# Kernel optimization log

Measured on AMD Instinct MI355X. Metric: run time of the kernel, lower is better.

The kernel has to match this reference:

```python
import jax, jax.numpy as jnp
import numpy as np

D_MODEL = 1024
N_HEADS = 16
N_GROUPS = 4
D_HEAD = D_MODEL // N_HEADS  # 64
HPG = N_HEADS // N_GROUPS    # heads per KV group = 4
B, T = 2, 2048


def _rope(x):
    # x: [B, H, T, D]; interleaved even/odd rotary, matching the torch module
    t, d = x.shape[2], x.shape[3]
    pos = jnp.arange(t, dtype=jnp.float32)[:, None]                      # [T,1]
    freq = jnp.exp(-(jnp.arange(0, d, 2, dtype=jnp.float32) / d)
                   * jnp.log(jnp.float32(10000.0)))                      # [D/2]
    angle = pos * freq                                                   # [T, D/2]
    cos, sin = jnp.cos(angle), jnp.sin(angle)
    xe, xo = x[..., ::2], x[..., 1::2]
    re = xe * cos - xo * sin
    ro = xe * sin + xo * cos
    return jnp.stack([re, ro], axis=-1).reshape(x.shape)


def setup_inputs() -> dict:
    key = jax.random.key(0)
    ks = jax.random.split(key, 10)
    s = 0.02
    return {
        "x":  jax.random.normal(ks[0], (B, T, D_MODEL), dtype=jnp.float32),
        "Wq": jax.random.normal(ks[1], (D_MODEL, D_MODEL), dtype=jnp.float32) * s,
        "bq": jax.random.normal(ks[2], (D_MODEL,), dtype=jnp.float32) * s,
        "Wk": jax.random.normal(ks[3], (D_MODEL, N_GROUPS * D_HEAD), dtype=jnp.float32) * s,
        "bk": jax.random.normal(ks[4], (N_GROUPS * D_HEAD,), dtype=jnp.float32) * s,
        "Wv": jax.random.normal(ks[5], (D_MODEL, N_GROUPS * D_HEAD), dtype=jnp.float32) * s,
        "bv": jax.random.normal(ks[6], (N_GROUPS * D_HEAD,), dtype=jnp.float32) * s,
        "Wo": jax.random.normal(ks[7], (D_MODEL, D_MODEL), dtype=jnp.float32) * s,
        "bo": jax.random.normal(ks[8], (D_MODEL,), dtype=jnp.float32) * s,
    }


def reference(x, Wq, bq, Wk, bk, Wv, bv, Wo, bo):
    b, t, _ = x.shape
    q = (x @ Wq + bq).reshape(b, t, N_HEADS, D_HEAD).transpose(0, 2, 1, 3)    # [B,H,T,D]
    k = (x @ Wk + bk).reshape(b, t, N_GROUPS, D_HEAD).transpose(0, 2, 1, 3)   # [B,G,T,D]
    v = (x @ Wv + bv).reshape(b, t, N_GROUPS, D_HEAD).transpose(0, 2, 1, 3)
    # GQA broadcast: idx = arange(n_heads) // heads_per_group  ==  repeat each group HPG times
    k = jnp.repeat(k, HPG, axis=1)                                            # [B,H,T,D]
    v = jnp.repeat(v, HPG, axis=1)
    q = _rope(q)
    k = _rope(k)
    scale = jnp.float32(np.sqrt(D_HEAD))
    scores = jnp.einsum('bhtd,bhsd->bhts', q, k) / scale                      # [B,H,T,T]
    causal = jnp.tril(jnp.ones((t, t), dtype=bool))
    scores = jnp.where(causal, scores, -jnp.inf)
    probs = jax.nn.softmax(scores, axis=-1)
    # dropout(p=0.05) is identity in eval mode
    attn = jnp.einsum('bhts,bhsd->bhtd', probs, v)
    out = attn.transpose(0, 2, 1, 3).reshape(b, t, N_HEADS * D_HEAD)
    return out @ Wo + bo
```

## Files before the change

### kernel.cpp

```cpp
#include <hip/hip_runtime.h>
#include <stdint.h>

typedef unsigned short u16;
typedef __attribute__((ext_vector_type(4))) float f32x4;
typedef __attribute__((ext_vector_type(8))) short bf16x8;
typedef __attribute__((ext_vector_type(4))) short bf16x4;

#define T_SEQ 2048
#define DM 1024
#define NH 16
#define NG 4
#define DH 64
#define QSCALE 0.18033688011112042f

__device__ __forceinline__ u16 f2bf(float f) {
    union { float f; uint32_t u; } v; v.f = f;
    uint32_t r = (v.u + 0x7FFFu + ((v.u >> 16) & 1u)) >> 16;
    return (u16)r;
}
__device__ __forceinline__ float bf2f(u16 u) {
    union { uint32_t u; float f; } v; v.u = ((uint32_t)u) << 16;
    return v.f;
}
__device__ __forceinline__ float fexp2(float x) {
#if __has_builtin(__builtin_amdgcn_exp2f)
    return __builtin_amdgcn_exp2f(x);
#else
    return exp2f(x);
#endif
}
__device__ __forceinline__ uint32_t cvtpk_bf16(float a, float b) {
    uint32_t r;
    asm("v_cvt_pk_bf16_f32 %0, %1, %2" : "=v"(r) : "v"(a), "v"(b));
    return r;
}

#if __has_builtin(__builtin_amdgcn_mfma_f32_16x16x16_bf16)
__device__ __forceinline__ f32x4 mfma16(bf16x4 a, bf16x4 b, f32x4 c) {
    return __builtin_amdgcn_mfma_f32_16x16x16_bf16(a, b, c, 0, 0, 0);
}
#elif __has_builtin(__builtin_amdgcn_mfma_f32_16x16x16bf16_1k)
__device__ __forceinline__ f32x4 mfma16(bf16x4 a, bf16x4 b, f32x4 c) {
    return __builtin_amdgcn_mfma_f32_16x16x16bf16_1k(a, b, c, 0, 0, 0);
}
#else
__device__ __forceinline__ f32x4 mfma16(bf16x4 a, bf16x4 b, f32x4 c) {
    asm("v_mfma_f32_16x16x16_bf16 %0, %1, %2, %0" : "+v"(c) : "v"(a), "v"(b));
    return c;
}
#endif

__device__ __forceinline__ void async16(const void* g, void* l) {
    __builtin_amdgcn_global_load_lds(
        (const __attribute__((address_space(1))) void*)g,
        (__attribute__((address_space(3))) void*)l,
        16, 0, 0);
}

__global__ __launch_bounds__(256) void k_prep(
    const float* __restrict__ x, u16* __restrict__ xb,
    const float* __restrict__ Wq, const float* __restrict__ Wk,
    const float* __restrict__ Wv, const float* __restrict__ Wo,
    u16* __restrict__ wqkvt, u16* __restrict__ wot,
    const float* __restrict__ bq, const float* __restrict__ bk,
    const float* __restrict__ bv, float* __restrict__ bqkv,
    float2* __restrict__ tbl) {
    int blk = blockIdx.x;
    int tid = threadIdx.x;
    if (blk < 2048) {
        int i = blk * 256 + tid;
        const float4* p = (const float4*)x + (size_t)i * 2;
        float4 a = p[0], b = p[1];
        bf16x8 v;
        v[0] = (short)f2bf(a.x); v[1] = (short)f2bf(a.y);
        v[2] = (short)f2bf(a.z); v[3] = (short)f2bf(a.w);
        v[4] = (short)f2bf(b.x); v[5] = (short)f2bf(b.y);
        v[6] = (short)f2bf(b.z); v[7] = (short)f2bf(b.w);
        ((bf16x8*)xb)[i] = v;
        return;
    }
    int t = blk - 2048;
    if (t >= 2560) {
        int u = t - 2560;
        if (u < 6) {
            int i = u * 256 + tid;
            if (i < 1536) {
                float v;
                if (i < 1024) v = bq[i];
                else if (i < 1280) v = bk[i - 1024];
                else v = bv[i - 1280];
                bqkv[i] = v;
            }
        } else {
            int idx = (u - 6) * 256 + tid;
            int tt = idx >> 5, i = idx & 31;
            float freq = exp2f(-(float)i * (13.287712379549449f / 32.0f));
            float ang = (float)tt * freq;
            tbl[idx] = make_float2(cosf(ang), sinf(ang));
        }
        return;
    }
    const float* src; u16* dst; int N;
    if (t < 1024)      { src = Wq; dst = wqkvt;                      N = 1024; }
    else if (t < 1280) { t -= 1024; src = Wk; dst = wqkvt + (size_t)1024 * 1024; N = 256; }
    else if (t < 1536) { t -= 1280; src = Wv; dst = wqkvt + (size_t)1280 * 1024; N = 256; }
    else               { t -= 1536; src = Wo; dst = wot;             N = 1024; }
    int ntiles = N >> 5;
    int n0 = (t % ntiles) * 32, k0 = (t / ntiles) * 32;
    __shared__ float tile[32][33];
    int tx = tid & 31, ty = tid >> 5;
#pragma unroll
    for (int q = 0; q < 4; q++)
        tile[ty + q * 8][tx] = src[(size_t)(k0 + ty + q * 8) * N + n0 + tx];
    __syncthreads();
#pragma unroll
    for (int q = 0; q < 4; q++)
        dst[(size_t)(n0 + ty + q * 8) * 1024 + k0 + tx] = f2bf(tile[tx][ty + q * 8]);
}

template <int B16OUT>
__global__ __launch_bounds__(256) void k_gemm_bt(
    const u16* __restrict__ A, const u16* __restrict__ Bt,
    const float* __restrict__ bias, void* __restrict__ Cv,
    int M, int N, int K) {
    __shared__ __align__(16) u16 As[64 * 64];
    __shared__ __align__(16) u16 Bs[128 * 64];
    int tid = threadIdx.x;
    int lane = tid & 63, wid = tid >> 6;
    int wr = wid >> 1, wc = wid & 1;
    int l15 = lane & 15, lhi = lane >> 4;
    int row0 = blockIdx.y * 64, col0 = blockIdx.x * 128;
    f32x4 acc[2][4] = {};

    for (int k0 = 0; k0 < K; k0 += 64) {
#pragma unroll
        for (int i = 0; i < 2; i++) {
            int c = i * 256 + tid;
            int r = c >> 3, ch = c & 7;
            int sch = ch ^ (r & 7);
            async16(A + (size_t)(row0 + r) * K + k0 + sch * 8, &As[c * 8]);
        }
#pragma unroll
        for (int i = 0; i < 4; i++) {
            int c = i * 256 + tid;
            int r = c >> 3, ch = c & 7;
            int sch = ch ^ (r & 7);
            async16(Bt + (size_t)(col0 + r) * K + k0 + sch * 8, &Bs[c * 8]);
        }
        __syncthreads();
#pragma unroll
        for (int ks = 0; ks < 2; ks++) {
            bf16x8 af[2], bfr[4];
#pragma unroll
            for (int m = 0; m < 2; m++) {
                int r = wr * 32 + m * 16 + l15;
                int kb = (ks * 64 + lhi * 16) ^ ((r & 7) << 4);
                af[m] = *(const bf16x8*)((const char*)As + r * 128 + kb);
            }
#pragma unroll
            for (int n = 0; n < 4; n++) {
                int r = wc * 64 + n * 16 + l15;
                int kb = (ks * 64 + lhi * 16) ^ ((r & 7) << 4);
                bfr[n] = *(const bf16x8*)((const char*)Bs + r * 128 + kb);
            }
#pragma unroll
            for (int m = 0; m < 2; m++)
#pragma unroll
                for (int n = 0; n < 4; n++)
                    acc[m][n] = __builtin_amdgcn_mfma_f32_16x16x32_bf16(
                        af[m], bfr[n], acc[m][n], 0, 0, 0);
        }
        __syncthreads();
    }
#pragma unroll
    for (int n = 0; n < 4; n++) {
        int col = col0 + wc * 64 + n * 16 + l15;
        float bv = bias[col];
#pragma unroll
        for (int m = 0; m < 2; m++) {
            int row = row0 + wr * 32 + m * 16 + lhi * 4;
#pragma unroll
            for (int i = 0; i < 4; i++) {
                float v = acc[m][n][i] + bv;
                if (B16OUT) ((u16*)Cv)[(size_t)(row + i) * N + col] = f2bf(v);
                else        ((float*)Cv)[(size_t)(row + i) * N + col] = v;
            }
        }
    }
}

__global__ __launch_bounds__(256) void k_rope_scatter(
    const u16* __restrict__ qkv, const float2* __restrict__ tbl,
    u16* __restrict__ Qo, u16* __restrict__ Ko, u16* __restrict__ Vto) {
    int bt = blockIdx.x;
    int t = bt & (T_SEQ - 1), b = bt >> 11;
    const u16* row = qkv + (size_t)bt * 1536;
    const uint32_t* row32 = (const uint32_t*)row;
    __shared__ float cs[32], sn[32];
    int tid = threadIdx.x;
    if (tid < 32) {
        float2 p = tbl[t * 32 + tid];
        cs[tid] = p.x; sn[tid] = p.y;
    }
    __syncthreads();
    for (int j = tid; j < 512; j += 256) {
        int i = j & 31;
        uint32_t w = row32[j];
        float xe = bf2f((u16)w), xo = bf2f((u16)(w >> 16));
        float c = cs[i], s = sn[i];
        float re = (xe * c - xo * s) * QSCALE;
        float ro = (xe * s + xo * c) * QSCALE;
        int hq = j >> 5;
        size_t base = (((size_t)(b * NH + hq)) * T_SEQ + t) * DH + 2 * i;
        Qo[base] = f2bf(re); Qo[base + 1] = f2bf(ro);
    }
    if (tid < 128) {
        int g = tid >> 5, i = tid & 31;
        uint32_t w = row32[512 + tid];
        float xe = bf2f((u16)w), xo = bf2f((u16)(w >> 16));
        float c = cs[i], s = sn[i];
        float re = xe * c - xo * s;
        float ro = xe * s + xo * c;
        size_t base = (((size_t)(b * NG + g)) * T_SEQ + t) * DH + 2 * i;
        Ko[base] = f2bf(re); Ko[base + 1] = f2bf(ro);
    }
    {
        int g = tid >> 6, d = tid & 63;
        Vto[(((size_t)(b * NG + g)) * DH + d) * T_SEQ + t] = row[1280 + tid];
    }
}

__global__ __launch_bounds__(256) void k_attn(
    const u16* __restrict__ Q, const u16* __restrict__ K,
    const u16* __restrict__ Vt, u16* __restrict__ Aout) {
    int i0 = blockIdx.x;
    int u = i0 >> 5;
    int qt = (u < 16) ? (31 - u) : (u - 16);
    int bh = i0 & 31;
    int b = bh >> 4, h = bh & 15, g = h >> 2;
    int tid = threadIdx.x;
    int lane = tid & 63, wid = tid >> 6;
    int l15 = lane & 15, lhi = lane >> 4;

    const u16* Kp = K + ((size_t)(b * NG + g)) * T_SEQ * DH;
    const u16* Vp = Vt + ((size_t)(b * NG + g)) * DH * T_SEQ;

    __shared__ __align__(16) u16 Ks[2][64 * 64];
    __shared__ __align__(16) u16 Vs[2][64 * 64];

    const u16* Qp = Q + ((size_t)bh * T_SEQ + qt * 64) * DH;
    bf16x8 qf[2];
#pragma unroll
    for (int ks = 0; ks < 2; ks++)
        qf[ks] = *(const bf16x8*)(Qp + (size_t)(wid * 16 + l15) * DH + ks * 32 + lhi * 8);

    f32x4 of[4] = {};
    float m_i = -3.0e38f, l_i = 0.f;

    int nt = qt + 1;
    int swz = (l15 & 7) << 4;

    int c0 = tid, c1 = tid + 256;
    int rk0 = c0 >> 3, sk0 = (c0 & 7) ^ (rk0 & 7);
    int rk1 = c1 >> 3, sk1 = (c1 & 7) ^ (rk1 & 7);
    const u16* kg0 = Kp + rk0 * DH + sk0 * 8;
    const u16* kg1 = Kp + rk1 * DH + sk1 * 8;
    const u16* vg0 = Vp + (size_t)rk0 * T_SEQ + sk0 * 8;
    const u16* vg1 = Vp + (size_t)rk1 * T_SEQ + sk1 * 8;

    async16(kg0, &Ks[0][c0 * 8]);
    async16(kg1, &Ks[0][c1 * 8]);
    async16(vg0, &Vs[0][c0 * 8]);
    async16(vg1, &Vs[0][c1 * 8]);
    __syncthreads();

#pragma unroll 1
    for (int it = 0; it < nt; it++) {
        int cur = it & 1;
        if (it + 1 < nt) {
            int nx = cur ^ 1;
            int ko = (it + 1) << 12;
            int vo = (it + 1) << 6;
            async16(kg0 + ko, &Ks[nx][c0 * 8]);
            async16(kg1 + ko, &Ks[nx][c1 * 8]);
            async16(vg0 + vo, &Vs[nx][c0 * 8]);
            async16(vg1 + vo, &Vs[nx][c1 * 8]);
        }
        const u16* Kc = Ks[cur];
        const u16* Vc = Vs[cur];

        f32x4 sf[4] = {};
        __builtin_amdgcn_s_setprio(1);
#pragma unroll
        for (int ks = 0; ks < 2; ks++)
#pragma unroll
            for (int n = 0; n < 4; n++) {
                int kb = (ks * 64 + lhi * 16) ^ swz;
                bf16x8 kf = *(const bf16x8*)((const char*)Kc + (n * 16 + l15) * 128 + kb);
                sf[n] = __builtin_amdgcn_mfma_f32_16x16x32_bf16(kf, qf[ks], sf[n], 0, 0, 0);
            }
        __builtin_amdgcn_s_setprio(0);

        if (it == nt - 1) {
            int qrow = qt * 64 + wid * 16 + l15;
            int sb = it * 64 + lhi * 4;
#pragma unroll
            for (int n = 0; n < 4; n++)
#pragma unroll
                for (int i = 0; i < 4; i++)
                    if (sb + n * 16 + i > qrow) sf[n][i] = -3.0e38f;
        }

        float pmt = sf[0][0];
#pragma unroll
        for (int n = 0; n < 4; n++)
#pragma unroll
            for (int i = 0; i < 4; i++)
                pmt = fmaxf(pmt, sf[n][i]);
        if (!__all(pmt - m_i <= 8.f)) {
#pragma unroll
            for (int off = 16; off <= 32; off <<= 1)
                pmt = fmaxf(pmt, __shfl_xor(pmt, off));
            float mn = fmaxf(m_i, pmt);
            float sc = fexp2(m_i - mn);
            m_i = mn;
            l_i *= sc;
            float sc4[4];
#pragma unroll
            for (int i = 0; i < 4; i++)
                sc4[i] = __shfl(sc, lhi * 4 + i);
#pragma unroll
            for (int n = 0; n < 4; n++)
#pragma unroll
                for (int i = 0; i < 4; i++)
                    of[n][i] *= sc4[i];
        }
        bf16x4 pa[4];
#pragma unroll
        for (int n = 0; n < 4; n++) {
#pragma unroll
            for (int i = 0; i < 4; i++) {
                float p = fexp2(sf[n][i] - m_i);
                sf[n][i] = p;
                l_i += p;
            }
            union { uint32_t u[2]; bf16x4 v; } pu;
            pu.u[0] = cvtpk_bf16(sf[n][0], sf[n][1]);
            pu.u[1] = cvtpk_bf16(sf[n][2], sf[n][3]);
            pa[n] = pu.v;
        }

        __builtin_amdgcn_s_setprio(1);
#pragma unroll
        for (int nd = 0; nd < 4; nd++) {
            int rowb = (nd * 16 + l15) * 128 + ((lhi & 1) << 3);
#pragma unroll
            for (int n = 0; n < 4; n++) {
                int cg = 2 * n + (lhi >> 1);
                int kb = ((cg << 4) ^ swz);
                bf16x4 vf = *(const bf16x4*)((const char*)Vc + rowb + kb);
                of[nd] = mfma16(pa[n], vf, of[nd]);
            }
        }
        __builtin_amdgcn_s_setprio(0);
        __syncthreads();
    }

#pragma unroll
    for (int off = 16; off <= 32; off <<= 1)
        l_i += __shfl_xor(l_i, off);
    float lq[4];
#pragma unroll
    for (int i = 0; i < 4; i++)
        lq[i] = __shfl(l_i, lhi * 4 + i);
#pragma unroll
    for (int n = 0; n < 4; n++)
#pragma unroll
        for (int i = 0; i < 4; i++) {
            int trow = qt * 64 + wid * 16 + lhi * 4 + i;
            float v = of[n][i] / lq[i];
            Aout[((size_t)(b * T_SEQ + trow)) * DM + h * 64 + n * 16 + l15] = f2bf(v);
        }
}

extern "C" void kernel_launch(void* const* d_in, const int* in_sizes, int n_in,
                              void* d_out, int out_size, void* d_ws, size_t ws_size,
                              hipStream_t stream) {
    const float* x  = (const float*)d_in[0];
    const float* Wq = (const float*)d_in[1];
    const float* bq = (const float*)d_in[2];
    const float* Wk = (const float*)d_in[3];
    const float* bk = (const float*)d_in[4];
    const float* Wv = (const float*)d_in[5];
    const float* bv = (const float*)d_in[6];
    const float* Wo = (const float*)d_in[7];
    const float* bo = (const float*)d_in[8];

    char* ws = (char*)d_ws;
    size_t o = 0;
    u16*   xb    = (u16*)(ws + o);  o += (size_t)4096 * 1024 * 2;
    u16*   wqkvt = (u16*)(ws + o);  o += (size_t)1536 * 1024 * 2;
    u16*   wot   = (u16*)(ws + o);  o += (size_t)1024 * 1024 * 2;
    float* bqkv  = (float*)(ws + o); o += 1536 * 4;
    o = (o + 255) & ~(size_t)255;
    u16*   qkvt  = (u16*)(ws + o);  o += (size_t)4096 * 1536 * 2;
    u16*   Qb    = (u16*)(ws + o);  o += (size_t)2 * NH * T_SEQ * DH * 2;
    u16*   Kb    = (u16*)(ws + o);  o += (size_t)2 * NG * T_SEQ * DH * 2;
    u16*   Vtb   = (u16*)(ws + o);  o += (size_t)2 * NG * DH * T_SEQ * 2;
    u16*   attnb = (u16*)(ws + o);  o += (size_t)4096 * 1024 * 2;
    float2* tbl  = (float2*)(ws + o); o += (size_t)2048 * 32 * 8;

    k_prep<<<4870, 256, 0, stream>>>(x, xb, Wq, Wk, Wv, Wo, wqkvt, wot, bq, bk, bv, bqkv, tbl);
    k_gemm_bt<1><<<dim3(12, 64), 256, 0, stream>>>(xb, wqkvt, bqkv, qkvt, 4096, 1536, 1024);
    k_rope_scatter<<<4096, 256, 0, stream>>>(qkvt, tbl, Qb, Kb, Vtb);
    k_attn<<<1024, 256, 0, stream>>>(Qb, Kb, Vtb, attnb);
    k_gemm_bt<0><<<dim3(8, 64), 256, 0, stream>>>(attnb, wot, bo, d_out, 4096, 1024, 1024);
}
```

Before: 101.5 us.

## Fuse RoPE and Q/K/V scatter into QKV GEMM epilogue, reswizzle V tile

Removes the separate rope/scatter kernel and the intermediate qkv buffer. The QKV GEMM epilogue now applies bias and RoPE, pairing even and odd columns with a lane shuffle, then writes Q, K and transposed V directly. Q is also scaled in this epilogue. The V layout in global memory and shared memory gets a new XOR swizzle, with matching address changes in the attention loads, to cut LDS bank conflicts. The cost is scattered 2-byte stores and per-element table loads in the GEMM epilogue.

```diff
diff --git a/kernel.cpp b/kernel.cpp
--- a/kernel.cpp
+++ b/kernel.cpp
@@ -118,10 +118,110 @@
         dst[(size_t)(n0 + ty + q * 8) * 1024 + k0 + tx] = f2bf(tile[tx][ty + q * 8]);
 }
 
-template <int B16OUT>
-__global__ __launch_bounds__(256) void k_gemm_bt(
+__global__ __launch_bounds__(256) void k_gemm_qkv(
     const u16* __restrict__ A, const u16* __restrict__ Bt,
-    const float* __restrict__ bias, void* __restrict__ Cv,
+    const float* __restrict__ bias, const float2* __restrict__ tbl,
+    u16* __restrict__ Qo, u16* __restrict__ Ko, u16* __restrict__ Vto) {
+    const int K = 1024;
+    __shared__ __align__(16) u16 As[64 * 64];
+    __shared__ __align__(16) u16 Bs[128 * 64];
+    int tid = threadIdx.x;
+    int lane = tid & 63, wid = tid >> 6;
+    int wr = wid >> 1, wc = wid & 1;
+    int l15 = lane & 15, lhi = lane >> 4;
+    int row0 = blockIdx.y * 64, col0 = blockIdx.x * 128;
+    f32x4 acc[2][4] = {};
+
+    for (int k0 = 0; k0 < K; k0 += 64) {
+#pragma unroll
+        for (int i = 0; i < 2; i++) {
+            int c = i * 256 + tid;
+            int r = c >> 3, ch = c & 7;
+            int sch = ch ^ (r & 7);
+            async16(A + (size_t)(row0 + r) * K + k0 + sch * 8, &As[c * 8]);
+        }
+#pragma unroll
+        for (int i = 0; i < 4; i++) {
+            int c = i * 256 + tid;
+            int r = c >> 3, ch = c & 7;
+            int sch = ch ^ (r & 7);
+            async16(Bt + (size_t)(col0 + r) * K + k0 + sch * 8, &Bs[c * 8]);
+        }
+        __syncthreads();
+#pragma unroll
+        for (int ks = 0; ks < 2; ks++) {
+            bf16x8 af[2], bfr[4];
+#pragma unroll
+            for (int m = 0; m < 2; m++) {
+                int r = wr * 32 + m * 16 + l15;
+                int kb = (ks * 64 + lhi * 16) ^ ((r & 7) << 4);
+                af[m] = *(const bf16x8*)((const char*)As + r * 128 + kb);
+            }
+#pragma unroll
+            for (int n = 0; n < 4; n++) {
+                int r = wc * 64 + n * 16 + l15;
+                int kb = (ks * 64 + lhi * 16) ^ ((r & 7) << 4);
+                bfr[n] = *(const bf16x8*)((const char*)Bs + r * 128 + kb);
+            }
+#pragma unroll
+            for (int m = 0; m < 2; m++)
+#pragma unroll
+                for (int n = 0; n < 4; n++)
+                    acc[m][n] = __builtin_amdgcn_mfma_f32_16x16x32_bf16(
+                        af[m], bfr[n], acc[m][n], 0, 0, 0);
+        }
+        __syncthreads();
+    }
+
+    int type = (col0 >= 1280) ? 2 : (col0 >= 1024 ? 1 : 0);
+    int rbase = row0 + wr * 32;
+#pragma unroll
+    for (int n = 0; n < 4; n++) {
+        int col = col0 + wc * 64 + n * 16 + l15;
+        float bv = bias[col];
+        if (type == 2) {
+            int cc = col - 1280;
+            int g = cc >> 6, d = cc & 63;
+#pragma unroll
+            for (int m = 0; m < 2; m++)
+#pragma unroll
+                for (int i = 0; i < 4; i++) {
+                    int rowg = rbase + m * 16 + lhi * 4 + i;
+                    int t = rowg & (T_SEQ - 1), b = rowg >> 11;
+                    int sp = t ^ ((d & 1) << 2);
+                    Vto[(((size_t)(b * NG + g)) * DH + d) * T_SEQ + sp] =
+                        f2bf(acc[m][n][i] + bv);
+                }
+        } else {
+            float ssgn = (col & 1) ? 1.f : -1.f;
+            int ip = (col & 63) >> 1;
+#pragma unroll
+            for (int m = 0; m < 2; m++)
+#pragma unroll
+                for (int i = 0; i < 4; i++) {
+                    int rowg = rbase + m * 16 + lhi * 4 + i;
+                    int t = rowg & (T_SEQ - 1), b = rowg >> 11;
+                    float v = acc[m][n][i] + bv;
+                    float other = __shfl_xor(v, 1);
+                    float2 cs = tbl[t * 32 + ip];
+                    float out = v * cs.x + other * cs.y * ssgn;
+                    if (type == 0) {
+                        int h = col >> 6, d = col & 63;
+                        Qo[(((size_t)(b * NH + h)) * T_SEQ + t) * DH + d] =
+                            f2bf(out * QSCALE);
+                    } else {
+                        int cc = col - 1024;
+                        int g = cc >> 6, d = cc & 63;
+                        Ko[(((size_t)(b * NG + g)) * T_SEQ + t) * DH + d] = f2bf(out);
+                    }
+                }
+        }
+    }
+}
+
+__global__ __launch_bounds__(256) void k_gemm_out(
+    const u16* __restrict__ A, const u16* __restrict__ Bt,
+    const float* __restrict__ bias, float* __restrict__ C,
     int M, int N, int K) {
     __shared__ __align__(16) u16 As[64 * 64];
     __shared__ __align__(16) u16 Bs[128 * 64];
@@ -180,53 +280,9 @@
         for (int m = 0; m < 2; m++) {
             int row = row0 + wr * 32 + m * 16 + lhi * 4;
 #pragma unroll
-            for (int i = 0; i < 4; i++) {
-                float v = acc[m][n][i] + bv;
-                if (B16OUT) ((u16*)Cv)[(size_t)(row + i) * N + col] = f2bf(v);
-                else        ((float*)Cv)[(size_t)(row + i) * N + col] = v;
-            }
-        }
-    }
-}
-
-__global__ __launch_bounds__(256) void k_rope_scatter(
-    const u16* __restrict__ qkv, const float2* __restrict__ tbl,
-    u16* __restrict__ Qo, u16* __restrict__ Ko, u16* __restrict__ Vto) {
-    int bt = blockIdx.x;
-    int t = bt & (T_SEQ - 1), b = bt >> 11;
-    const u16* row = qkv + (size_t)bt * 1536;
-    const uint32_t* row32 = (const uint32_t*)row;
-    __shared__ float cs[32], sn[32];
-    int tid = threadIdx.x;
-    if (tid < 32) {
-        float2 p = tbl[t * 32 + tid];
-        cs[tid] = p.x; sn[tid] = p.y;
-    }
-    __syncthreads();
-    for (int j = tid; j < 512; j += 256) {
-        int i = j & 31;
-        uint32_t w = row32[j];
-        float xe = bf2f((u16)w), xo = bf2f((u16)(w >> 16));
-        float c = cs[i], s = sn[i];
-        float re = (xe * c - xo * s) * QSCALE;
-        float ro = (xe * s + xo * c) * QSCALE;
-        int hq = j >> 5;
-        size_t base = (((size_t)(b * NH + hq)) * T_SEQ + t) * DH + 2 * i;
-        Qo[base] = f2bf(re); Qo[base + 1] = f2bf(ro);
-    }
-    if (tid < 128) {
-        int g = tid >> 5, i = tid & 31;
-        uint32_t w = row32[512 + tid];
-        float xe = bf2f((u16)w), xo = bf2f((u16)(w >> 16));
-        float c = cs[i], s = sn[i];
-        float re = xe * c - xo * s;
-        float ro = xe * s + xo * c;
-        size_t base = (((size_t)(b * NG + g)) * T_SEQ + t) * DH + 2 * i;
-        Ko[base] = f2bf(re); Ko[base + 1] = f2bf(ro);
-    }
-    {
-        int g = tid >> 6, d = tid & 63;
-        Vto[(((size_t)(b * NG + g)) * DH + d) * T_SEQ + t] = row[1280 + tid];
+            for (int i = 0; i < 4; i++)
+                C[(size_t)(row + i) * N + col] = acc[m][n][i] + bv;
+        }
     }
 }
 
@@ -261,12 +317,15 @@
     int swz = (l15 & 7) << 4;
 
     int c0 = tid, c1 = tid + 256;
-    int rk0 = c0 >> 3, sk0 = (c0 & 7) ^ (rk0 & 7);
-    int rk1 = c1 >> 3, sk1 = (c1 & 7) ^ (rk1 & 7);
+    int rk0 = c0 >> 3, rk1 = c1 >> 3;
+    int sk0 = (c0 & 7) ^ (rk0 & 7);
+    int sk1 = (c1 & 7) ^ (rk1 & 7);
+    int sv0 = (c0 & 7) ^ ((rk0 >> 1) & 7);
+    int sv1 = (c1 & 7) ^ ((rk1 >> 1) & 7);
     const u16* kg0 = Kp + rk0 * DH + sk0 * 8;
     const u16* kg1 = Kp + rk1 * DH + sk1 * 8;
-    const u16* vg0 = Vp + (size_t)rk0 * T_SEQ + sk0 * 8;
-    const u16* vg1 = Vp + (size_t)rk1 * T_SEQ + sk1 * 8;
+    const u16* vg0 = Vp + (size_t)rk0 * T_SEQ + sv0 * 8;
+    const u16* vg1 = Vp + (size_t)rk1 * T_SEQ + sv1 * 8;
 
     async16(kg0, &Ks[0][c0 * 8]);
     async16(kg1, &Ks[0][c1 * 8]);
@@ -353,11 +412,10 @@
         __builtin_amdgcn_s_setprio(1);
 #pragma unroll
         for (int nd = 0; nd < 4; nd++) {
-            int rowb = (nd * 16 + l15) * 128 + ((lhi & 1) << 3);
+            int rowb = (nd * 16 + l15) * 128;
 #pragma unroll
             for (int n = 0; n < 4; n++) {
-                int cg = 2 * n + (lhi >> 1);
-                int kb = ((cg << 4) ^ swz);
+                int kb = ((4 * n + lhi) ^ l15) << 3;
                 bf16x4 vf = *(const bf16x4*)((const char*)Vc + rowb + kb);
                 of[nd] = mfma16(pa[n], vf, of[nd]);
             }
@@ -403,7 +461,6 @@
     u16*   wot   = (u16*)(ws + o);  o += (size_t)1024 * 1024 * 2;
     float* bqkv  = (float*)(ws + o); o += 1536 * 4;
     o = (o + 255) & ~(size_t)255;
-    u16*   qkvt  = (u16*)(ws + o);  o += (size_t)4096 * 1536 * 2;
     u16*   Qb    = (u16*)(ws + o);  o += (size_t)2 * NH * T_SEQ * DH * 2;
     u16*   Kb    = (u16*)(ws + o);  o += (size_t)2 * NG * T_SEQ * DH * 2;
     u16*   Vtb   = (u16*)(ws + o);  o += (size_t)2 * NG * DH * T_SEQ * 2;
@@ -411,8 +468,7 @@
     float2* tbl  = (float2*)(ws + o); o += (size_t)2048 * 32 * 8;
 
     k_prep<<<4870, 256, 0, stream>>>(x, xb, Wq, Wk, Wv, Wo, wqkvt, wot, bq, bk, bv, bqkv, tbl);
-    k_gemm_bt<1><<<dim3(12, 64), 256, 0, stream>>>(xb, wqkvt, bqkv, qkvt, 4096, 1536, 1024);
-    k_rope_scatter<<<4096, 256, 0, stream>>>(qkvt, tbl, Qb, Kb, Vtb);
+    k_gemm_qkv<<<dim3(12, 64), 256, 0, stream>>>(xb, wqkvt, bqkv, tbl, Qb, Kb, Vtb);
     k_attn<<<1024, 256, 0, stream>>>(Qb, Kb, Vtb, attnb);
-    k_gemm_bt<0><<<dim3(8, 64), 256, 0, stream>>>(attnb, wot, bo, d_out, 4096, 1024, 1024);
-}
+    k_gemm_out<<<dim3(8, 64), 256, 0, stream>>>(attnb, wot, bo, (float*)d_out, 4096, 1024, 1024);
+}
```

New measurement: 91.30 us. 10.1% less time.
